# Optimization experiments

Hardware: AMD Instinct MI355X
Metric: run time of the kernel (lower is better)

The kernel has to match this reference:

```python
import jax, jax.numpy as jnp
import numpy as np

TEMPERATURE = 8.0  # sqrt(head_dim=64)


def setup_inputs() -> dict:
    key = jax.random.key(0)
    kq, kk, kv, km = jax.random.split(key, 4)
    B, S, D = 16, 2048, 64
    q = jax.random.normal(kq, (B, S, D), dtype=jnp.float32)
    k = jax.random.normal(kk, (B, S, D), dtype=jnp.float32)
    v = jax.random.normal(kv, (B, S, D), dtype=jnp.float32)
    mask = jax.random.randint(km, (B, S, S), 0, 2).astype(jnp.bool_)
    return {"q": q, "k": k, "v": v, "mask": mask}


def reference(q, k, v, mask):
    # latent = q @ k^T / temperature  -> [B, Sq, Sk]
    latent = jnp.einsum('bqd,bkd->bqk', q, k) / TEMPERATURE
    # NOTE: the original fills masked positions with 1e-9 (NOT -inf); keep faithful.
    latent = jnp.where(mask, jnp.float32(1e-9), latent)
    attn = jax.nn.softmax(latent, axis=-1)
    return jnp.einsum('bqk,bkd->bqd', attn, v)
```

## Files before the change

### kernel.cpp

```cpp
#include <hip/hip_runtime.h>
#include <hip/hip_bf16.h>

#define BB 16
#define SS 2048
#define DD 64

typedef __attribute__((ext_vector_type(8)))  unsigned short ushort8;
typedef __attribute__((ext_vector_type(8)))  __bf16 bf16x8;
typedef __attribute__((ext_vector_type(4)))  float f32x4;

static __device__ __forceinline__ unsigned short f2bf(float x) {
    return __builtin_bit_cast(unsigned short, __float2bfloat16(x));
}
static __device__ __forceinline__ unsigned pk2(float a, float b) {
    return (unsigned)f2bf(a) | ((unsigned)f2bf(b) << 16);
}
union F4 { float4 v; float a[4]; };

__global__ void sdpa_detect_mask_mode(const unsigned int* __restrict__ m,
                                      int* __restrict__ mode_out) {
    __shared__ int s01, sfl;
    const int t = threadIdx.x;
    if (t == 0) { s01 = 1; sfl = 1; }
    __syncthreads();
    unsigned int v = m[t];
    if (!(v == 0u || v == 1u)) atomicAnd(&s01, 0);
    if (!(v == 0u || v == 0x3F800000u)) atomicAnd(&sfl, 0);
    __syncthreads();
    if (t == 0) *mode_out = s01 ? 1 : (sfl ? 2 : 0);
}

__global__ __launch_bounds__(256, 2)
void sdpa_mfma16_kernel(const float* __restrict__ Q, const float* __restrict__ K,
                        const float* __restrict__ V, const void* __restrict__ M,
                        float* __restrict__ O, const int* __restrict__ modep) {
    __shared__ __align__(16) char Qs[8192];
    __shared__ __align__(16) char Ks[8192];
    __shared__ __align__(16) char Vt[8192];
    __shared__ __align__(16) char Ps[8192];
    __shared__ __align__(16) unsigned char Ms[64 * 72];

    const int t    = threadIdx.x;
    const int lane = t & 63;
    const int l15  = lane & 15;
    const int quad = lane >> 4;
    const int w    = t >> 6;
    const int b    = blockIdx.y;
    const int q0   = blockIdx.x * 64;
    const int mode = *modep;

    const float* Kg = K + (size_t)b * SS * DD;
    const float* Vg = V + (size_t)b * SS * DD;

    const int sr = t >> 2;
    const int sc = t & 3;

    {
        const float* src = Q + ((size_t)b * SS + q0 + sr) * DD + sc * 16;
        F4 f0, f1, f2, f3;
        f0.v = *(const float4*)(src);
        f1.v = *(const float4*)(src + 4);
        f2.v = *(const float4*)(src + 8);
        f3.v = *(const float4*)(src + 12);
        ushort8 u0, u1;
        #pragma unroll
        for (int e = 0; e < 4; e++) {
            u0[e]     = f2bf(f0.a[e] * 0.125f);
            u0[e + 4] = f2bf(f1.a[e] * 0.125f);
            u1[e]     = f2bf(f2.a[e] * 0.125f);
            u1[e + 4] = f2bf(f3.a[e] * 0.125f);
        }
        *(ushort8*)(Qs + sr * 128 + (((2 * sc)     ^ (sr & 7)) * 16)) = u0;
        *(ushort8*)(Qs + sr * 128 + (((2 * sc + 1) ^ (sr & 7)) * 16)) = u1;
    }
    __syncthreads();

    bf16x8 aq[2];
    {
        const int qrow = 16 * w + l15;
        #pragma unroll
        for (int c = 0; c < 2; c++)
            aq[c] = __builtin_bit_cast(bf16x8, *(const ushort8*)(
                Qs + qrow * 128 + (((4 * c + quad) ^ (qrow & 7)) * 16)));
    }

    f32x4 acc[4];
    #pragma unroll
    for (int dc = 0; dc < 4; dc++)
        #pragma unroll
        for (int r = 0; r < 4; r++) acc[dc][r] = 0.f;
    float den_r[4] = {0.f, 0.f, 0.f, 0.f};

    const int d0v = (t & 15) * 4;
    const int kkb = (t >> 4) * 2;

    for (int kt = 0; kt < SS / 64; ++kt) {
        {
            const float* src = Kg + (size_t)(kt * 64 + sr) * DD + sc * 16;
            F4 f0, f1, f2, f3;
            f0.v = *(const float4*)(src);
            f1.v = *(const float4*)(src + 4);
            f2.v = *(const float4*)(src + 8);
            f3.v = *(const float4*)(src + 12);
            ushort8 u0, u1;
            #pragma unroll
            for (int e = 0; e < 4; e++) {
                u0[e]     = f2bf(f0.a[e]);
                u0[e + 4] = f2bf(f1.a[e]);
                u1[e]     = f2bf(f2.a[e]);
                u1[e + 4] = f2bf(f3.a[e]);
            }
            *(ushort8*)(Ks + sr * 128 + (((2 * sc)     ^ (sr & 7)) * 16)) = u0;
            *(ushort8*)(Ks + sr * 128 + (((2 * sc + 1) ^ (sr & 7)) * 16)) = u1;
        }
        #pragma unroll
        for (int it2 = 0; it2 < 2; it2++) {
            const int kk = kkb + 32 * it2;
            F4 va, vb;
            va.v = *(const float4*)(Vg + (size_t)(kt * 64 + kk)     * DD + d0v);
            vb.v = *(const float4*)(Vg + (size_t)(kt * 64 + kk + 1) * DD + d0v);
            #pragma unroll
            for (int e = 0; e < 4; e++) {
                const int d = d0v + e;
                *(unsigned*)(Vt + d * 128 + (((kk >> 3) ^ (d & 7)) * 16) + (kk & 7) * 2)
                    = pk2(va.a[e], vb.a[e]);
            }
        }
        if (mode == 0) {
            const unsigned char* Mb = (const unsigned char*)M +
                (size_t)b * SS * SS + (size_t)(q0 + sr) * SS + kt * 64 + sc * 16;
            const uint4 mv = *(const uint4*)Mb;
            *(uint2*)(Ms + sr * 72 + sc * 16)     = make_uint2(mv.x, mv.y);
            *(uint2*)(Ms + sr * 72 + sc * 16 + 8) = make_uint2(mv.z, mv.w);
        } else {
            const unsigned int* Mw = (const unsigned int*)M +
                (size_t)b * SS * SS + (size_t)(q0 + sr) * SS + kt * 64 + sc * 16;
            unsigned wd[4];
            #pragma unroll
            for (int g = 0; g < 4; g++) {
                const uint4 u = *(const uint4*)(Mw + 4 * g);
                wd[g] = (u.x ? 1u : 0u) | (u.y ? 0x100u : 0u) |
                        (u.z ? 0x10000u : 0u) | (u.w ? 0x1000000u : 0u);
            }
            *(uint2*)(Ms + sr * 72 + sc * 16)     = make_uint2(wd[0], wd[1]);
            *(uint2*)(Ms + sr * 72 + sc * 16 + 8) = make_uint2(wd[2], wd[3]);
        }
        __syncthreads();

        #pragma unroll
        for (int kc = 0; kc < 4; kc++) {
            f32x4 S;
            #pragma unroll
            for (int r = 0; r < 4; r++) S[r] = 0.f;
            const int krow = 16 * kc + l15;
            #pragma unroll
            for (int c = 0; c < 2; c++) {
                bf16x8 bk = __builtin_bit_cast(bf16x8, *(const ushort8*)(
                    Ks + krow * 128 + (((4 * c + quad) ^ (krow & 7)) * 16)));
                S = __builtin_amdgcn_mfma_f32_16x16x32_bf16(aq[c], bk, S, 0, 0, 0);
            }
            #pragma unroll
            for (int r = 0; r < 4; r++) {
                const int qq = 4 * quad + r;
                const unsigned char mb = Ms[(16 * w + qq) * 72 + 16 * kc + l15];
                const float ev = __expf(S[r]);
                const float pv = mb ? 1.0f : ev;
                den_r[r] += pv;
                const int col = 16 * kc + l15;
                *(unsigned short*)(Ps + w * 2048 + qq * 128 +
                    (((col >> 3) ^ (qq & 7)) * 16) + (col & 7) * 2) = f2bf(pv);
            }
        }

        #pragma unroll
        for (int kc2 = 0; kc2 < 2; kc2++) {
            bf16x8 ap = __builtin_bit_cast(bf16x8, *(const ushort8*)(
                Ps + w * 2048 + l15 * 128 + (((4 * kc2 + quad) ^ (l15 & 7)) * 16)));
            #pragma unroll
            for (int dc = 0; dc < 4; dc++) {
                const int vrow = 16 * dc + l15;
                bf16x8 bv = __builtin_bit_cast(bf16x8, *(const ushort8*)(
                    Vt + vrow * 128 + (((4 * kc2 + quad) ^ (vrow & 7)) * 16)));
                acc[dc] = __builtin_amdgcn_mfma_f32_16x16x32_bf16(ap, bv, acc[dc], 0, 0, 0);
            }
        }
        __syncthreads();
    }

    #pragma unroll
    for (int m = 1; m <= 8; m <<= 1)
        #pragma unroll
        for (int r = 0; r < 4; r++)
            den_r[r] += __shfl_xor(den_r[r], m, 64);

    #pragma unroll
    for (int r = 0; r < 4; r++) {
        const int qg = q0 + 16 * w + 4 * quad + r;
        const float inv = 1.0f / den_r[r];
        float* Og = O + ((size_t)b * SS + qg) * DD;
        #pragma unroll
        for (int dc = 0; dc < 4; dc++)
            Og[16 * dc + l15] = acc[dc][r] * inv;
    }
}

extern "C" void kernel_launch(void* const* d_in, const int* in_sizes, int n_in,
                              void* d_out, int out_size, void* d_ws, size_t ws_size,
                              hipStream_t stream) {
    const float* q = (const float*)d_in[0];
    const float* k = (const float*)d_in[1];
    const float* v = (const float*)d_in[2];
    const void*  m = d_in[3];
    float* out = (float*)d_out;
    int* mode = (int*)d_ws;

    sdpa_detect_mask_mode<<<1, 256, 0, stream>>>((const unsigned int*)m, mode);

    dim3 grid(SS / 64, BB);
    sdpa_mfma16_kernel<<<grid, 256, 0, stream>>>(q, k, v, m, out, mode);
}
```

Measured before the change: 408.8 us.

## Switch to 32x32x16 MFMA with register-resident P and split-K warp reduction

Replaces 16x16 MFMA tiles with 32x32x16 MFMA, splitting warps into two query halves and two key halves. The probabilities now stay in registers and are exchanged with cross-lane shuffles instead of going through an LDS round trip, and the two key-half partial outputs are combined through shared memory at the end. It also drops the mask-mode detection kernel and always reads the mask as 32-bit words, which removes a launch but assumes that mask format.

```diff
diff --git a/kernel.cpp b/kernel.cpp
--- a/kernel.cpp
+++ b/kernel.cpp
@@ -7,7 +7,7 @@
 
 typedef __attribute__((ext_vector_type(8)))  unsigned short ushort8;
 typedef __attribute__((ext_vector_type(8)))  __bf16 bf16x8;
-typedef __attribute__((ext_vector_type(4)))  float f32x4;
+typedef __attribute__((ext_vector_type(16))) float f32x16;
 
 static __device__ __forceinline__ unsigned short f2bf(float x) {
     return __builtin_bit_cast(unsigned short, __float2bfloat16(x));
@@ -15,49 +15,42 @@
 static __device__ __forceinline__ unsigned pk2(float a, float b) {
     return (unsigned)f2bf(a) | ((unsigned)f2bf(b) << 16);
 }
+
 union F4 { float4 v; float a[4]; };
 
-__global__ void sdpa_detect_mask_mode(const unsigned int* __restrict__ m,
-                                      int* __restrict__ mode_out) {
-    __shared__ int s01, sfl;
-    const int t = threadIdx.x;
-    if (t == 0) { s01 = 1; sfl = 1; }
-    __syncthreads();
-    unsigned int v = m[t];
-    if (!(v == 0u || v == 1u)) atomicAnd(&s01, 0);
-    if (!(v == 0u || v == 0x3F800000u)) atomicAnd(&sfl, 0);
-    __syncthreads();
-    if (t == 0) *mode_out = s01 ? 1 : (sfl ? 2 : 0);
-}
-
 __global__ __launch_bounds__(256, 2)
-void sdpa_mfma16_kernel(const float* __restrict__ Q, const float* __restrict__ K,
-                        const float* __restrict__ V, const void* __restrict__ M,
-                        float* __restrict__ O, const int* __restrict__ modep) {
-    __shared__ __align__(16) char Qs[8192];
-    __shared__ __align__(16) char Ks[8192];
-    __shared__ __align__(16) char Vt[8192];
-    __shared__ __align__(16) char Ps[8192];
-    __shared__ __align__(16) unsigned char Ms[64 * 72];
+void sdpa_mfma_kernel(const float* __restrict__ Q, const float* __restrict__ K,
+                      const float* __restrict__ V, const unsigned int* __restrict__ M,
+                      float* __restrict__ O) {
+    __shared__ __align__(16) char smem[29184];
+    char* Qs = smem;
+    char* Ks = smem + 8192;
+    char* Vs = smem + 16384;
+    char* Ms = smem + 24576;
+    float* red  = (float*)(smem + 8192);
+    float* denx = (float*)(smem + 24576);
 
     const int t    = threadIdx.x;
     const int lane = t & 63;
-    const int l15  = lane & 15;
-    const int quad = lane >> 4;
+    const int l31  = lane & 31;
+    const int half = lane >> 5;
     const int w    = t >> 6;
+    const int qs   = w & 1;
+    const int kh   = w >> 1;
     const int b    = blockIdx.y;
     const int q0   = blockIdx.x * 64;
-    const int mode = *modep;
-
+
+    const float* Qg = Q + ((size_t)b * SS + q0) * DD;
     const float* Kg = K + (size_t)b * SS * DD;
     const float* Vg = V + (size_t)b * SS * DD;
+    const unsigned int* Mg = M + (size_t)b * SS * SS + (size_t)q0 * SS;
 
     const int sr = t >> 2;
     const int sc = t & 3;
 
     {
-        const float* src = Q + ((size_t)b * SS + q0 + sr) * DD + sc * 16;
         F4 f0, f1, f2, f3;
+        const float* src = Qg + sr * DD + sc * 16;
         f0.v = *(const float4*)(src);
         f1.v = *(const float4*)(src + 4);
         f2.v = *(const float4*)(src + 8);
@@ -70,34 +63,30 @@
             u1[e]     = f2bf(f2.a[e] * 0.125f);
             u1[e + 4] = f2bf(f3.a[e] * 0.125f);
         }
-        *(ushort8*)(Qs + sr * 128 + (((2 * sc)     ^ (sr & 7)) * 16)) = u0;
-        *(ushort8*)(Qs + sr * 128 + (((2 * sc + 1) ^ (sr & 7)) * 16)) = u1;
+        *(ushort8*)(Qs + sr * 128 + (((sc * 2)     ^ (sr & 7)) * 16)) = u0;
+        *(ushort8*)(Qs + sr * 128 + (((sc * 2 + 1) ^ (sr & 7)) * 16)) = u1;
     }
     __syncthreads();
 
-    bf16x8 aq[2];
-    {
-        const int qrow = 16 * w + l15;
-        #pragma unroll
-        for (int c = 0; c < 2; c++)
-            aq[c] = __builtin_bit_cast(bf16x8, *(const ushort8*)(
-                Qs + qrow * 128 + (((4 * c + quad) ^ (qrow & 7)) * 16)));
-    }
-
-    f32x4 acc[4];
+    const int qrow = 32 * qs + l31;
+    ushort8 bq[4];
     #pragma unroll
     for (int dc = 0; dc < 4; dc++)
-        #pragma unroll
-        for (int r = 0; r < 4; r++) acc[dc][r] = 0.f;
-    float den_r[4] = {0.f, 0.f, 0.f, 0.f};
-
-    const int d0v = (t & 15) * 4;
-    const int kkb = (t >> 4) * 2;
+        bq[dc] = *(const ushort8*)(Qs + qrow * 128 + (((2 * dc + half) ^ (qrow & 7)) * 16));
+
+    f32x16 On0, On1;
+    #pragma unroll
+    for (int i = 0; i < 16; i++) { On0[i] = 0.f; On1[i] = 0.f; }
+    float den_acc = 0.f;
+
+    const int krow = 32 * kh + l31;
+    const int d0v  = (t & 15) * 4;
+    const int kkb  = (t >> 4) * 2;
 
     for (int kt = 0; kt < SS / 64; ++kt) {
         {
+            F4 f0, f1, f2, f3;
             const float* src = Kg + (size_t)(kt * 64 + sr) * DD + sc * 16;
-            F4 f0, f1, f2, f3;
             f0.v = *(const float4*)(src);
             f1.v = *(const float4*)(src + 4);
             f2.v = *(const float4*)(src + 8);
@@ -110,31 +99,26 @@
                 u1[e]     = f2bf(f2.a[e]);
                 u1[e + 4] = f2bf(f3.a[e]);
             }
-            *(ushort8*)(Ks + sr * 128 + (((2 * sc)     ^ (sr & 7)) * 16)) = u0;
-            *(ushort8*)(Ks + sr * 128 + (((2 * sc + 1) ^ (sr & 7)) * 16)) = u1;
-        }
-        #pragma unroll
-        for (int it2 = 0; it2 < 2; it2++) {
-            const int kk = kkb + 32 * it2;
-            F4 va, vb;
-            va.v = *(const float4*)(Vg + (size_t)(kt * 64 + kk)     * DD + d0v);
-            vb.v = *(const float4*)(Vg + (size_t)(kt * 64 + kk + 1) * DD + d0v);
-            #pragma unroll
-            for (int e = 0; e < 4; e++) {
-                const int d = d0v + e;
-                *(unsigned*)(Vt + d * 128 + (((kk >> 3) ^ (d & 7)) * 16) + (kk & 7) * 2)
-                    = pk2(va.a[e], vb.a[e]);
-            }
-        }
-        if (mode == 0) {
-            const unsigned char* Mb = (const unsigned char*)M +
-                (size_t)b * SS * SS + (size_t)(q0 + sr) * SS + kt * 64 + sc * 16;
-            const uint4 mv = *(const uint4*)Mb;
-            *(uint2*)(Ms + sr * 72 + sc * 16)     = make_uint2(mv.x, mv.y);
-            *(uint2*)(Ms + sr * 72 + sc * 16 + 8) = make_uint2(mv.z, mv.w);
-        } else {
-            const unsigned int* Mw = (const unsigned int*)M +
-                (size_t)b * SS * SS + (size_t)(q0 + sr) * SS + kt * 64 + sc * 16;
+            *(ushort8*)(Ks + sr * 128 + (((sc * 2)     ^ (sr & 7)) * 16)) = u0;
+            *(ushort8*)(Ks + sr * 128 + (((sc * 2 + 1) ^ (sr & 7)) * 16)) = u1;
+        }
+        {
+            #pragma unroll
+            for (int it2 = 0; it2 < 2; it2++) {
+                const int kk = kkb + 32 * it2;
+                F4 va, vb;
+                va.v = *(const float4*)(Vg + (size_t)(kt * 64 + kk)     * DD + d0v);
+                vb.v = *(const float4*)(Vg + (size_t)(kt * 64 + kk + 1) * DD + d0v);
+                #pragma unroll
+                for (int e = 0; e < 4; e++) {
+                    const int d = d0v + e;
+                    *(unsigned*)(Vs + d * 128 + (((kk >> 3) ^ (d & 7)) * 16) + (kk & 7) * 2)
+                        = pk2(va.a[e], vb.a[e]);
+                }
+            }
+        }
+        {
+            const unsigned int* Mw = Mg + (size_t)sr * SS + kt * 64 + sc * 16;
             unsigned wd[4];
             #pragma unroll
             for (int g = 0; g < 4; g++) {
@@ -147,60 +131,92 @@
         }
         __syncthreads();
 
-        #pragma unroll
-        for (int kc = 0; kc < 4; kc++) {
-            f32x4 S;
-            #pragma unroll
-            for (int r = 0; r < 4; r++) S[r] = 0.f;
-            const int krow = 16 * kc + l15;
-            #pragma unroll
-            for (int c = 0; c < 2; c++) {
-                bf16x8 bk = __builtin_bit_cast(bf16x8, *(const ushort8*)(
-                    Ks + krow * 128 + (((4 * c + quad) ^ (krow & 7)) * 16)));
-                S = __builtin_amdgcn_mfma_f32_16x16x32_bf16(aq[c], bk, S, 0, 0, 0);
-            }
-            #pragma unroll
-            for (int r = 0; r < 4; r++) {
-                const int qq = 4 * quad + r;
-                const unsigned char mb = Ms[(16 * w + qq) * 72 + 16 * kc + l15];
-                const float ev = __expf(S[r]);
-                const float pv = mb ? 1.0f : ev;
-                den_r[r] += pv;
-                const int col = 16 * kc + l15;
-                *(unsigned short*)(Ps + w * 2048 + qq * 128 +
-                    (((col >> 3) ^ (qq & 7)) * 16) + (col & 7) * 2) = f2bf(pv);
-            }
-        }
-
-        #pragma unroll
-        for (int kc2 = 0; kc2 < 2; kc2++) {
-            bf16x8 ap = __builtin_bit_cast(bf16x8, *(const ushort8*)(
-                Ps + w * 2048 + l15 * 128 + (((4 * kc2 + quad) ^ (l15 & 7)) * 16)));
-            #pragma unroll
-            for (int dc = 0; dc < 4; dc++) {
-                const int vrow = 16 * dc + l15;
-                bf16x8 bv = __builtin_bit_cast(bf16x8, *(const ushort8*)(
-                    Vt + vrow * 128 + (((4 * kc2 + quad) ^ (vrow & 7)) * 16)));
-                acc[dc] = __builtin_amdgcn_mfma_f32_16x16x32_bf16(ap, bv, acc[dc], 0, 0, 0);
+        f32x16 S;
+        #pragma unroll
+        for (int i = 0; i < 16; i++) S[i] = 0.f;
+        #pragma unroll
+        for (int dc = 0; dc < 4; dc++) {
+            bf16x8 ak = __builtin_bit_cast(bf16x8,
+                *(const ushort8*)(Ks + krow * 128 + (((2 * dc + half) ^ (krow & 7)) * 16)));
+            S = __builtin_amdgcn_mfma_f32_32x32x16_bf16(
+                    ak, __builtin_bit_cast(bf16x8, bq[dc]), S, 0, 0, 0);
+        }
+
+        float p[16];
+        #pragma unroll
+        for (int g = 0; g < 4; g++) {
+            const unsigned mw = *(const unsigned*)(Ms + qrow * 72 + 32 * kh + 8 * g + 4 * half);
+            #pragma unroll
+            for (int e = 0; e < 4; e++) {
+                const float ev = __expf(S[4 * g + e]);
+                const float pv = ((mw >> (8 * e)) & 0xffu) ? 1.0f : ev;
+                p[4 * g + e] = pv;
+                den_acc += pv;
+            }
+        }
+
+        #pragma unroll
+        for (int s2 = 0; s2 < 2; s2++) {
+            const unsigned o0 = pk2(p[8 * s2 + 0], p[8 * s2 + 1]);
+            const unsigned o1 = pk2(p[8 * s2 + 2], p[8 * s2 + 3]);
+            const unsigned o2 = pk2(p[8 * s2 + 4], p[8 * s2 + 5]);
+            const unsigned o3 = pk2(p[8 * s2 + 6], p[8 * s2 + 7]);
+            const unsigned s0 = half ? o0 : o2;
+            const unsigned s1 = half ? o1 : o3;
+            const unsigned r0 = (unsigned)__shfl_xor((int)s0, 32, 64);
+            const unsigned r1 = (unsigned)__shfl_xor((int)s1, 32, 64);
+            uint4 bu;
+            bu.x = half ? r0 : o0;
+            bu.y = half ? r1 : o1;
+            bu.z = half ? o2 : r0;
+            bu.w = half ? o3 : r1;
+            const bf16x8 bp = __builtin_bit_cast(bf16x8, bu);
+            #pragma unroll
+            for (int dc = 0; dc < 2; dc++) {
+                const int vrow = 32 * dc + l31;
+                bf16x8 av = __builtin_bit_cast(bf16x8,
+                    *(const ushort8*)(Vs + vrow * 128 +
+                        (((4 * kh + 2 * s2 + half) ^ (vrow & 7)) * 16)));
+                if (dc == 0) On0 = __builtin_amdgcn_mfma_f32_32x32x16_bf16(av, bp, On0, 0, 0, 0);
+                else         On1 = __builtin_amdgcn_mfma_f32_32x32x16_bf16(av, bp, On1, 0, 0, 0);
             }
         }
         __syncthreads();
     }
 
-    #pragma unroll
-    for (int m = 1; m <= 8; m <<= 1)
-        #pragma unroll
-        for (int r = 0; r < 4; r++)
-            den_r[r] += __shfl_xor(den_r[r], m, 64);
-
-    #pragma unroll
-    for (int r = 0; r < 4; r++) {
-        const int qg = q0 + 16 * w + 4 * quad + r;
-        const float inv = 1.0f / den_r[r];
-        float* Og = O + ((size_t)b * SS + qg) * DD;
-        #pragma unroll
-        for (int dc = 0; dc < 4; dc++)
-            Og[16 * dc + l15] = acc[dc][r] * inv;
+    const float den_tot = den_acc + __shfl_xor(den_acc, 32, 64);
+
+    __syncthreads();
+    if (kh == 1) {
+        #pragma unroll
+        for (int dc = 0; dc < 2; dc++)
+            #pragma unroll
+            for (int g = 0; g < 4; g++) {
+                const f32x16& Oc = dc ? On1 : On0;
+                float4 st;
+                st.x = Oc[4 * g + 0]; st.y = Oc[4 * g + 1];
+                st.z = Oc[4 * g + 2]; st.w = Oc[4 * g + 3];
+                *(float4*)((char*)red + qs * 8192 + (dc * 4 + g) * 1024 + lane * 16) = st;
+            }
+        if (lane < 32) denx[qs * 32 + l31] = den_tot;
+    }
+    __syncthreads();
+    if (kh == 0) {
+        const float inv = 1.0f / (den_tot + denx[qs * 32 + l31]);
+        float* Og = O + ((size_t)b * SS + q0 + qrow) * DD;
+        #pragma unroll
+        for (int dc = 0; dc < 2; dc++)
+            #pragma unroll
+            for (int g = 0; g < 4; g++) {
+                const float4 pr = *(const float4*)((char*)red + qs * 8192 + (dc * 4 + g) * 1024 + lane * 16);
+                const f32x16& Oc = dc ? On1 : On0;
+                float4 st;
+                st.x = (Oc[4 * g + 0] + pr.x) * inv;
+                st.y = (Oc[4 * g + 1] + pr.y) * inv;
+                st.z = (Oc[4 * g + 2] + pr.z) * inv;
+                st.w = (Oc[4 * g + 3] + pr.w) * inv;
+                *(float4*)(Og + 32 * dc + 8 * g + 4 * half) = st;
+            }
     }
 }
 
@@ -210,12 +226,9 @@
     const float* q = (const float*)d_in[0];
     const float* k = (const float*)d_in[1];
     const float* v = (const float*)d_in[2];
-    const void*  m = d_in[3];
+    const unsigned int* m = (const unsigned int*)d_in[3];
     float* out = (float*)d_out;
-    int* mode = (int*)d_ws;
-
-    sdpa_detect_mask_mode<<<1, 256, 0, stream>>>((const unsigned int*)m, mode);
 
     dim3 grid(SS / 64, BB);
-    sdpa_mfma16_kernel<<<grid, 256, 0, stream>>>(q, k, v, m, out, mode);
-}
+    sdpa_mfma_kernel<<<grid, 256, 0, stream>>>(q, k, v, m, out);
+}
```

New measurement: 473.3 us. 1.16x slower.
